# Performance work log

Measured on AMD Instinct MI355X. Metric: run time of the kernel, lower is better.

Reference implementation:

```python
import jax, jax.numpy as jnp
import numpy as np

N = 50000   # nodes per graph
E = 800000  # edges per graph
D = 128     # in_dim (num_features)
H = 128     # hidden_channels
R = 8       # num_etypes


def setup_inputs() -> dict:
    key = jax.random.key(0)
    ks = jax.random.split(key, 32)
    inp = {}
    inp["x1"] = jax.random.normal(ks[0], (N, D), dtype=jnp.float32)
    inp["edge_index1"] = jax.random.randint(ks[1], (2, E), 0, N)
    inp["edge_type1"] = jnp.sort(jax.random.randint(ks[2], (E,), 0, R))
    inp["x2"] = jax.random.normal(ks[3], (N, D), dtype=jnp.float32)
    inp["edge_index2"] = jax.random.randint(ks[4], (2, E), 0, N)
    inp["edge_type2"] = jnp.sort(jax.random.randint(ks[5], (E,), 0, R))
    # RGCNConv params: relation weights [R, in, out], root weight [in, out], bias [out]
    dims = [(D, H), (H, H), (H, H)]
    k = 6
    for l, (di, do) in enumerate(dims):
        s = 1.0 / np.sqrt(di)
        inp[f"W{l}"] = jax.random.normal(ks[k], (R, di, do), dtype=jnp.float32) * s; k += 1
        inp[f"root{l}"] = jax.random.normal(ks[k], (di, do), dtype=jnp.float32) * s; k += 1
        inp[f"bias{l}"] = jnp.zeros((do,), dtype=jnp.float32)
    # FCL: MLP on concat(u1, u2) of width 2*H -> H -> 1 (assumed architecture)
    s = 1.0 / np.sqrt(2 * H)
    inp["fc1_w"] = jax.random.normal(ks[k], (2 * H, H), dtype=jnp.float32) * s; k += 1
    inp["fc1_b"] = jnp.zeros((H,), dtype=jnp.float32)
    s = 1.0 / np.sqrt(H)
    inp["fc2_w"] = jax.random.normal(ks[k], (H, 1), dtype=jnp.float32) * s; k += 1
    inp["fc2_b"] = jnp.zeros((1,), dtype=jnp.float32)
    return inp


def rgcn_conv(x, src, dst, etype, W, root, bias):
    # PyG RGCNConv: out_i = root @ x_i + bias + sum_r mean_{j in N_r(i)} W_r x_j
    # transform all nodes by all relation weights: [R, N, H]
    t = jnp.einsum('nd,rdh->rnh', x, W)
    msg = t[etype, src]                       # [E, H] per-edge gathered messages
    comb = dst * R + etype                    # combined (node, relation) segment id
    cnt = jax.ops.segment_sum(jnp.ones((E,), x.dtype), comb, num_segments=N * R)
    msg = msg * (1.0 / jnp.maximum(cnt, 1.0))[comb][:, None]  # per-relation mean norm
    agg = jax.ops.segment_sum(msg, dst, num_segments=N)       # scatter-add over relations
    return agg + x @ root + bias


def gnn(x, edge_index, edge_type, params):
    src, dst = edge_index[0], edge_index[1]
    u = jax.nn.relu(rgcn_conv(x, src, dst, edge_type, *params[0]))
    u = jax.nn.relu(rgcn_conv(u, src, dst, edge_type, *params[1]))
    u = rgcn_conv(u, src, dst, edge_type, *params[2])
    return jnp.mean(u, axis=0).reshape(1, -1)  # [1, H]


def reference(x1, edge_index1, edge_type1, x2, edge_index2, edge_type2,
              W0, root0, bias0, W1, root1, bias1, W2, root2, bias2,
              fc1_w, fc1_b, fc2_w, fc2_b):
    params = [(W0, root0, bias0), (W1, root1, bias1), (W2, root2, bias2)]
    u1 = gnn(x1, edge_index1, edge_type1, params)
    u2 = gnn(x2, edge_index2, edge_type2, params)
    h = jnp.concatenate([u1, u2], axis=-1)    # [1, 2H]
    return jax.nn.relu(h @ fc1_w + fc1_b) @ fc2_w + fc2_b  # [1, 1]
```

## Files before the change

kernel.cpp:

```cpp
#include <hip/hip_runtime.h>

#define R_ET 8
#define DH 128

typedef __bf16 bf16x8 __attribute__((ext_vector_type(8)));
typedef float f32x4 __attribute__((ext_vector_type(4)));

__device__ __forceinline__ ushort f2bf(float f) {
  unsigned u = __float_as_uint(f);
  u += 0x7fff + ((u >> 16) & 1);
  return (ushort)(u >> 16);
}


__global__ void count_kernel(const int* __restrict__ ei, const int* __restrict__ et,
                             int* __restrict__ cnt, int E) {
  int e = blockIdx.x * blockDim.x + threadIdx.x;
  if (e < E) atomicAdd(&cnt[ei[E + e] * R_ET + et[e]], 1);
}

__global__ __launch_bounds__(1024) void scan1_kernel(const int* __restrict__ cnt,
                                                     int* __restrict__ off,
                                                     int* __restrict__ bsum, int N) {
  __shared__ int s[1024];
  int tid = threadIdx.x;
  int node = blockIdx.x * 1024 + tid;
  int d = 0;
  if (node < N) {
    const int4* c = (const int4*)&cnt[node * R_ET];
    int4 a = c[0], b = c[1];
    d = a.x + a.y + a.z + a.w + b.x + b.y + b.z + b.w;
  }
  s[tid] = d;
  __syncthreads();
  for (int step = 1; step < 1024; step <<= 1) {
    int v = (tid >= step) ? s[tid - step] : 0;
    __syncthreads();
    s[tid] += v;
    __syncthreads();
  }
  if (node < N) off[node] = s[tid] - d;
  if (tid == 1023) bsum[blockIdx.x] = s[1023];
}

__global__ __launch_bounds__(1024) void scan2_kernel(int* __restrict__ bsum, int nb) {
  __shared__ int s[1024];
  int tid = threadIdx.x;
  int v = (tid < nb) ? bsum[tid] : 0;
  s[tid] = v;
  __syncthreads();
  for (int step = 1; step < 1024; step <<= 1) {
    int x = (tid >= step) ? s[tid - step] : 0;
    __syncthreads();
    s[tid] += x;
    __syncthreads();
  }
  if (tid < nb) bsum[tid] = s[tid] - v;
}

__global__ __launch_bounds__(1024) void scan3_kernel(int* __restrict__ off,
                                                     int* __restrict__ cursor,
                                                     const int* __restrict__ bsum,
                                                     int N, int E) {
  int node = blockIdx.x * 1024 + threadIdx.x;
  if (node < N) {
    int o = off[node] + bsum[blockIdx.x];
    off[node] = o;
    cursor[node] = o;
  }
  if (node == 0) off[N] = E;
}

__global__ void place_kernel(const int* __restrict__ ei, const int* __restrict__ et,
                             const int* __restrict__ cnt, int* __restrict__ cursor,
                             int2* __restrict__ meta, int E) {
  int e = blockIdx.x * blockDim.x + threadIdx.x;
  if (e >= E) return;
  int src = ei[e], dst = ei[E + e], r = et[e];
  int slot = atomicAdd(&cursor[dst], 1);
  meta[slot] = make_int2(src | (r << 28),
                         __float_as_int(1.f / (float)cnt[dst * R_ET + r]));
}

__global__ __launch_bounds__(256) void wconv_kernel(const float* __restrict__ root,
                                                    const float* __restrict__ W,
                                                    ushort* __restrict__ Wt) {
  int mat = blockIdx.x;
  const float* src = (mat == 0) ? root : (W + (size_t)(mat - 1) * DH * DH);
  ushort* dst = Wt + (size_t)mat * DH * DH;
  for (int idx = threadIdx.x; idx < DH * DH; idx += 256) {
    int n = idx >> 7, k = idx & 127;
    dst[n * DH + (((k >> 3) ^ (n & 7)) << 3) + (k & 7)] = f2bf(src[k * DH + n]);
  }
}

__global__ __launch_bounds__(256) void aconv_kernel(const float* __restrict__ src,
                                                    ushort* __restrict__ dst,
                                                    int total, int padtotal) {
  int i4 = (blockIdx.x * 256 + threadIdx.x) * 4;
  if (i4 >= padtotal) return;
  int row = i4 >> 7, k = i4 & 127;
  ushort4 o = make_ushort4(0, 0, 0, 0);
  if (i4 < total) {
    float4 v = *(const float4*)&src[i4];
    o = make_ushort4(f2bf(v.x), f2bf(v.y), f2bf(v.z), f2bf(v.w));
  }
  *(ushort4*)&dst[(size_t)row * DH + (((k >> 3) ^ (row & 7)) << 3) + (k & 7)] = o;
}

__global__ __launch_bounds__(256) void gemm_mfma(
    const ushort* __restrict__ Abf, const ushort* __restrict__ Wt,
    const float* __restrict__ bias, float* __restrict__ y,
    ushort* __restrict__ t, int N) {
  __shared__ ushort As[128 * DH];
  __shared__ ushort Bs[128 * DH];
  const int tid = threadIdx.x;
  const int wave = tid >> 6, lane = tid & 63;
  const int quad = lane >> 4, l15 = lane & 15;
  const int rbase = blockIdx.x * 128;
  const int wr = (wave >> 1) * 64, wc = (wave & 1) * 64;

  const ushort* gA = Abf + (size_t)rbase * DH;
#pragma unroll
  for (int it = 0; it < 8; it++) {
    __builtin_amdgcn_global_load_lds(
        (const __attribute__((address_space(1))) void*)(gA + (it * 256 + tid) * 8),
        (__attribute__((address_space(3))) void*)(As + (it * 256 + wave * 64) * 8), 16, 0, 0);
  }
  {
    const ushort* gB = Wt + (size_t)(blockIdx.y * 3) * DH * DH;
#pragma unroll
    for (int it = 0; it < 8; it++) {
      __builtin_amdgcn_global_load_lds(
          (const __attribute__((address_space(1))) void*)(gB + (it * 256 + tid) * 8),
          (__attribute__((address_space(3))) void*)(Bs + (it * 256 + wave * 64) * 8), 16, 0, 0);
    }
  }

  for (int m = 0; m < 3; m++) {
    const int mat = blockIdx.y * 3 + m;
    __syncthreads();

    f32x4 acc[4][4];
#pragma unroll
    for (int i = 0; i < 4; i++)
#pragma unroll
      for (int j = 0; j < 4; j++) acc[i][j] = (f32x4){0.f, 0.f, 0.f, 0.f};

#pragma unroll
    for (int kc = 0; kc < 4; kc++) {
      bf16x8 af[4], bfr[4];
#pragma unroll
      for (int i = 0; i < 4; i++) {
        int ra = wr + i * 16 + l15;
        int rb = wc + i * 16 + l15;
        af[i] = *(const bf16x8*)&As[ra * DH + (((kc * 4 + quad) ^ (ra & 7)) << 3)];
        bfr[i] = *(const bf16x8*)&Bs[rb * DH + (((kc * 4 + quad) ^ (rb & 7)) << 3)];
      }
#pragma unroll
      for (int i = 0; i < 4; i++)
#pragma unroll
        for (int j = 0; j < 4; j++)
          acc[i][j] = __builtin_amdgcn_mfma_f32_16x16x32_bf16(bfr[j], af[i], acc[i][j], 0, 0, 0);
    }

    if (m < 2) {
      __syncthreads();
      const ushort* gB = Wt + (size_t)(mat + 1) * DH * DH;
#pragma unroll
      for (int it = 0; it < 8; it++) {
        __builtin_amdgcn_global_load_lds(
            (const __attribute__((address_space(1))) void*)(gB + (it * 256 + tid) * 8),
            (__attribute__((address_space(3))) void*)(Bs + (it * 256 + wave * 64) * 8), 16, 0, 0);
      }
    }

    if (mat == 0) {
#pragma unroll
      for (int i = 0; i < 4; i++) {
        int node = rbase + wr + i * 16 + l15;
        if (node < N) {
#pragma unroll
          for (int j = 0; j < 4; j++) {
            int c0 = wc + j * 16 + quad * 4;
            float4 bv = *(const float4*)&bias[c0];
            float4 v = make_float4(acc[i][j][0] + bv.x, acc[i][j][1] + bv.y,
                                   acc[i][j][2] + bv.z, acc[i][j][3] + bv.w);
            *(float4*)&y[(size_t)node * DH + c0] = v;
          }
        }
      }
    } else {
      ushort* tp = t + (size_t)(mat - 1) * (size_t)N * DH;
#pragma unroll
      for (int i = 0; i < 4; i++) {
        int node = rbase + wr + i * 16 + l15;
        if (node < N) {
#pragma unroll
          for (int j = 0; j < 4; j++) {
            int c0 = wc + j * 16 + quad * 4;
            unsigned lo = (unsigned)f2bf(acc[i][j][0]) | ((unsigned)f2bf(acc[i][j][1]) << 16);
            unsigned hi = (unsigned)f2bf(acc[i][j][2]) | ((unsigned)f2bf(acc[i][j][3]) << 16);
            *(uint2*)&tp[(size_t)node * DH + c0] = make_uint2(lo, hi);
          }
        }
      }
    }
  }
}

__device__ __forceinline__ void gather_accum(const int2* __restrict__ meta,
                                             const ushort* __restrict__ t,
                                             int start, int end, int lane, int N,
                                             float& ax, float& ay) {
  const int colb = lane * 2;
  for (int base = start; base < end; base += 64) {
    int m = min(64, end - base);
    int2 md = make_int2(0, 0);
    if (lane < m) md = meta[base + lane];
    int j = 0;
    for (; j + 4 <= m; j += 4) {
      int p0 = __shfl(md.x, j),     q0 = __shfl(md.y, j);
      int p1 = __shfl(md.x, j + 1), q1 = __shfl(md.y, j + 1);
      int p2 = __shfl(md.x, j + 2), q2 = __shfl(md.y, j + 2);
      int p3 = __shfl(md.x, j + 3), q3 = __shfl(md.y, j + 3);
      unsigned u0 = *(const unsigned*)&t[(((size_t)((unsigned)p0 >> 28) * N + (p0 & 0x0fffffff)) << 7) + colb];
      unsigned u1 = *(const unsigned*)&t[(((size_t)((unsigned)p1 >> 28) * N + (p1 & 0x0fffffff)) << 7) + colb];
      unsigned u2 = *(const unsigned*)&t[(((size_t)((unsigned)p2 >> 28) * N + (p2 & 0x0fffffff)) << 7) + colb];
      unsigned u3 = *(const unsigned*)&t[(((size_t)((unsigned)p3 >> 28) * N + (p3 & 0x0fffffff)) << 7) + colb];
      float s0 = __int_as_float(q0), s1 = __int_as_float(q1);
      float s2 = __int_as_float(q2), s3 = __int_as_float(q3);
      ax = fmaf(__uint_as_float(u0 << 16), s0, ax);
      ay = fmaf(__uint_as_float(u0 & 0xffff0000u), s0, ay);
      ax = fmaf(__uint_as_float(u1 << 16), s1, ax);
      ay = fmaf(__uint_as_float(u1 & 0xffff0000u), s1, ay);
      ax = fmaf(__uint_as_float(u2 << 16), s2, ax);
      ay = fmaf(__uint_as_float(u2 & 0xffff0000u), s2, ay);
      ax = fmaf(__uint_as_float(u3 << 16), s3, ax);
      ay = fmaf(__uint_as_float(u3 & 0xffff0000u), s3, ay);
    }
    for (; j < m; j++) {
      int pj = __shfl(md.x, j);
      float sj = __int_as_float(__shfl(md.y, j));
      unsigned u = *(const unsigned*)&t[(((size_t)((unsigned)pj >> 28) * N + (pj & 0x0fffffff)) << 7) + colb];
      ax = fmaf(__uint_as_float(u << 16), sj, ax);
      ay = fmaf(__uint_as_float(u & 0xffff0000u), sj, ay);
    }
  }
}

__global__ __launch_bounds__(256) void gather_mid(
    const int* __restrict__ off, const int2* __restrict__ meta,
    const ushort* __restrict__ t, const float* __restrict__ y,
    ushort* __restrict__ Abf, int N) {
  int dst = blockIdx.x * 4 + (threadIdx.x >> 6);
  if (dst >= N) return;
  int lane = threadIdx.x & 63;
  float ax = 0.f, ay = 0.f;
  gather_accum(meta, t, off[dst], off[dst + 1], lane, N, ax, ay);
  float2 yv = *(const float2*)&y[(size_t)dst * DH + lane * 2];
  float rx = fmaxf(yv.x + ax, 0.f);
  float ry = fmaxf(yv.y + ay, 0.f);
  unsigned o = (unsigned)f2bf(rx) | ((unsigned)f2bf(ry) << 16);
  int k = lane * 2;
  *(unsigned*)&Abf[(size_t)dst * DH + (((k >> 3) ^ (dst & 7)) << 3) + (k & 7)] = o;
}

__global__ __launch_bounds__(256) void gather_last(
    const int* __restrict__ off, const int2* __restrict__ meta,
    const ushort* __restrict__ t, float* __restrict__ y, int N) {
  int dst = blockIdx.x * 4 + (threadIdx.x >> 6);
  if (dst >= N) return;
  int lane = threadIdx.x & 63;
  float ax = 0.f, ay = 0.f;
  gather_accum(meta, t, off[dst], off[dst + 1], lane, N, ax, ay);
  float2* yp = (float2*)&y[(size_t)dst * DH + lane * 2];
  float2 yv = *yp;
  yv.x += ax;
  yv.y += ay;
  *yp = yv;
}

__global__ __launch_bounds__(256) void pool_kernel(const float* __restrict__ y,
                                                   float* __restrict__ u, int N) {
  __shared__ float s[256];
  int tid = threadIdx.x;
  int c = tid & 127, rr = tid >> 7;
  int n0 = blockIdx.x * 100;
  int nend = min(n0 + 100, N);
  float sum = 0.f;
  for (int n = n0 + rr; n < nend; n += 2) sum += y[(size_t)n * DH + c];
  s[tid] = sum;
  __syncthreads();
  if (tid < 128) atomicAdd(&u[c], s[tid] + s[tid + 128]);
}

__global__ __launch_bounds__(256) void mlp_kernel(
    const float* __restrict__ u, const float* __restrict__ fc1w,
    const float* __restrict__ fc1b, const float* __restrict__ fc2w,
    const float* __restrict__ fc2b, float* __restrict__ out, int N) {
  __shared__ float uin[256];
  __shared__ float hred[128];
  int tid = threadIdx.x;
  uin[tid] = u[tid] * (1.f / (float)N);
  __syncthreads();
  if (tid < 128) {
    float s = fc1b[tid];
    for (int i = 0; i < 256; i++) s = fmaf(uin[i], fc1w[i * 128 + tid], s);
    s = fmaxf(s, 0.f);
    hred[tid] = s * fc2w[tid];
  }
  __syncthreads();
  if (tid == 0) {
    float s = fc2b[0];
    for (int i = 0; i < 128; i++) s += hred[i];
    out[0] = s;
  }
}

extern "C" void kernel_launch(void* const* d_in, const int* in_sizes, int n_in,
                              void* d_out, int out_size, void* d_ws, size_t ws_size,
                              hipStream_t stream) {
  const float* x[2] = {(const float*)d_in[0], (const float*)d_in[3]};
  const int* ei[2] = {(const int*)d_in[1], (const int*)d_in[4]};
  const int* et[2] = {(const int*)d_in[2], (const int*)d_in[5]};
  const float* Wp[3] = {(const float*)d_in[6], (const float*)d_in[9], (const float*)d_in[12]};
  const float* rootp[3] = {(const float*)d_in[7], (const float*)d_in[10], (const float*)d_in[13]};
  const float* biasp[3] = {(const float*)d_in[8], (const float*)d_in[11], (const float*)d_in[14]};
  const float* fc1w = (const float*)d_in[15];
  const float* fc1b = (const float*)d_in[16];
  const float* fc2w = (const float*)d_in[17];
  const float* fc2b = (const float*)d_in[18];

  const int N = in_sizes[0] / DH;
  const int E = in_sizes[2];
  const int Npad = (N + 127) & ~127;
  const int NB = (N + 1023) / 1024;

  char* ws = (char*)d_ws;
  size_t ob = 0;
  auto alloc = [&](size_t bytes) {
    void* p = ws + ob;
    ob = (ob + bytes + 255) & ~(size_t)255;
    return p;
  };
  float* y = (float*)alloc((size_t)N * DH * 4);
  int* cnt = (int*)alloc((size_t)N * R_ET * 4);
  int* offs = (int*)alloc((size_t)(N + 1) * 4);
  int* cursor = (int*)alloc((size_t)N * 4);
  int* bsum = (int*)alloc(1024 * 4);
  int2* meta = (int2*)alloc((size_t)E * 8);
  float* u = (float*)alloc(1024);
  ushort* Abf = (ushort*)alloc((size_t)Npad * DH * 2);
  ushort* Wt = (ushort*)alloc((size_t)3 * 9 * DH * DH * 2);
  ushort* tbuf = (ushort*)alloc((size_t)R_ET * N * DH * 2);
  (void)ws_size;

  hipMemsetAsync(u, 0, 2 * DH * sizeof(float), stream);
  for (int l = 0; l < 3; l++)
    wconv_kernel<<<9, 256, 0, stream>>>(rootp[l], Wp[l], Wt + (size_t)l * 9 * DH * DH);

  dim3 ggrid(Npad / 128, 3);
  dim3 egrid((E + 255) / 256);
  dim3 ngrid((N + 3) / 4);
  const int total = N * DH, padtotal = Npad * DH;
  dim3 agrid((padtotal / 4 + 255) / 256);

  for (int g = 0; g < 2; g++) {
    hipMemsetAsync(cnt, 0, (size_t)N * R_ET * sizeof(int), stream);
    count_kernel<<<egrid, 256, 0, stream>>>(ei[g], et[g], cnt, E);
    scan1_kernel<<<NB, 1024, 0, stream>>>(cnt, offs, bsum, N);
    scan2_kernel<<<1, 1024, 0, stream>>>(bsum, NB);
    scan3_kernel<<<NB, 1024, 0, stream>>>(offs, cursor, bsum, N, E);
    place_kernel<<<egrid, 256, 0, stream>>>(ei[g], et[g], cnt, cursor, meta, E);
    aconv_kernel<<<agrid, 256, 0, stream>>>(x[g], Abf, total, padtotal);
    for (int l = 0; l < 3; l++) {
      gemm_mfma<<<ggrid, 256, 0, stream>>>(Abf, Wt + (size_t)l * 9 * DH * DH,
                                           biasp[l], y, tbuf, N);
      if (l < 2) {
        gather_mid<<<ngrid, 256, 0, stream>>>(offs, meta, tbuf, y, Abf, N);
      } else {
        gather_last<<<ngrid, 256, 0, stream>>>(offs, meta, tbuf, y, N);
      }
    }
    pool_kernel<<<(N + 99) / 100, 256, 0, stream>>>(y, u + g * DH, N);
  }
  mlp_kernel<<<1, 256, 0, stream>>>(u, fc1w, fc1b, fc2w, fc2b, (float*)d_out, N);
}
```

Before: 895.7 us.

## Build CSR with two-level bucket sort and fuse final gather with mean pooling

Replaces the per-(node,relation) global count, three-kernel scan and global-cursor placement with a coarse bucket count over 128-node buckets, a single-block scan, a coarse scatter, and a per-bucket shared-memory sort that also computes the per-relation mean normalisation. The last-layer gather now adds the root term and accumulates the pooled sum directly, removing the y write-back and the separate pool kernel. This reduces global atomics and launches for graph preprocessing but adds many global atomics onto 128 pooled addresses from every block.

```diff
diff --git a/kernel.cpp b/kernel.cpp
--- a/kernel.cpp
+++ b/kernel.cpp
@@ -13,73 +13,97 @@
 }
 
 
-__global__ void count_kernel(const int* __restrict__ ei, const int* __restrict__ et,
-                             int* __restrict__ cnt, int E) {
+
+__global__ void coarse_count(const int* __restrict__ ei, int* __restrict__ bcnt, int E) {
   int e = blockIdx.x * blockDim.x + threadIdx.x;
-  if (e < E) atomicAdd(&cnt[ei[E + e] * R_ET + et[e]], 1);
-}
-
-__global__ __launch_bounds__(1024) void scan1_kernel(const int* __restrict__ cnt,
-                                                     int* __restrict__ off,
-                                                     int* __restrict__ bsum, int N) {
+  if (e < E) atomicAdd(&bcnt[ei[E + e] >> 7], 1);
+}
+
+__global__ __launch_bounds__(1024) void coarse_scan(const int* __restrict__ bcnt,
+                                                    int* __restrict__ bbase,
+                                                    int* __restrict__ bcur,
+                                                    int nb, int E) {
   __shared__ int s[1024];
   int tid = threadIdx.x;
-  int node = blockIdx.x * 1024 + tid;
-  int d = 0;
-  if (node < N) {
-    const int4* c = (const int4*)&cnt[node * R_ET];
-    int4 a = c[0], b = c[1];
-    d = a.x + a.y + a.z + a.w + b.x + b.y + b.z + b.w;
-  }
-  s[tid] = d;
-  __syncthreads();
-  for (int step = 1; step < 1024; step <<= 1) {
-    int v = (tid >= step) ? s[tid - step] : 0;
-    __syncthreads();
-    s[tid] += v;
-    __syncthreads();
-  }
-  if (node < N) off[node] = s[tid] - d;
-  if (tid == 1023) bsum[blockIdx.x] = s[1023];
-}
-
-__global__ __launch_bounds__(1024) void scan2_kernel(int* __restrict__ bsum, int nb) {
-  __shared__ int s[1024];
-  int tid = threadIdx.x;
-  int v = (tid < nb) ? bsum[tid] : 0;
+  int v = (tid < nb) ? bcnt[tid] : 0;
   s[tid] = v;
   __syncthreads();
-  for (int step = 1; step < 1024; step <<= 1) {
-    int x = (tid >= step) ? s[tid - step] : 0;
+  for (int st = 1; st < 1024; st <<= 1) {
+    int x = (tid >= st) ? s[tid - st] : 0;
     __syncthreads();
     s[tid] += x;
     __syncthreads();
   }
-  if (tid < nb) bsum[tid] = s[tid] - v;
-}
-
-__global__ __launch_bounds__(1024) void scan3_kernel(int* __restrict__ off,
-                                                     int* __restrict__ cursor,
-                                                     const int* __restrict__ bsum,
-                                                     int N, int E) {
-  int node = blockIdx.x * 1024 + threadIdx.x;
-  if (node < N) {
-    int o = off[node] + bsum[blockIdx.x];
-    off[node] = o;
-    cursor[node] = o;
-  }
-  if (node == 0) off[N] = E;
-}
-
-__global__ void place_kernel(const int* __restrict__ ei, const int* __restrict__ et,
-                             const int* __restrict__ cnt, int* __restrict__ cursor,
-                             int2* __restrict__ meta, int E) {
+  if (tid < nb) {
+    bbase[tid] = s[tid] - v;
+    bcur[tid] = s[tid] - v;
+  }
+  if (tid == 0) bbase[nb] = E;
+}
+
+__global__ void coarse_place(const int* __restrict__ ei, const int* __restrict__ et,
+                             int* __restrict__ bcur, int* __restrict__ ebuf, int E) {
   int e = blockIdx.x * blockDim.x + threadIdx.x;
   if (e >= E) return;
   int src = ei[e], dst = ei[E + e], r = et[e];
-  int slot = atomicAdd(&cursor[dst], 1);
-  meta[slot] = make_int2(src | (r << 28),
-                         __float_as_int(1.f / (float)cnt[dst * R_ET + r]));
+  int slot = atomicAdd(&bcur[dst >> 7], 1);
+  ebuf[slot] = src | (r << 16) | ((dst & 127) << 19);
+}
+
+__global__ __launch_bounds__(256) void bucket_sort(
+    const int* __restrict__ bbase, const int* __restrict__ ebuf,
+    int2* __restrict__ meta, int* __restrict__ off, int N, int E) {
+  __shared__ int hist[1024];
+  __shared__ int cur[1024];
+  __shared__ float inv[1024];
+  __shared__ int tsum[256];
+  const int b = blockIdx.x, tid = threadIdx.x;
+  const int s0 = bbase[b], s1 = bbase[b + 1];
+
+  for (int k = tid; k < 1024; k += 256) hist[k] = 0;
+  __syncthreads();
+  for (int i = s0 + tid; i < s1; i += 256) {
+    int e = ebuf[i];
+    atomicAdd(&hist[(e >> 16) & 1023], 1);
+  }
+  __syncthreads();
+
+  const int base4 = tid * 4;
+  int h0 = hist[base4], h1 = hist[base4 + 1], h2 = hist[base4 + 2], h3 = hist[base4 + 3];
+  int s = h0 + h1 + h2 + h3;
+  tsum[tid] = s;
+  __syncthreads();
+  for (int st = 1; st < 256; st <<= 1) {
+    int x = (tid >= st) ? tsum[tid - st] : 0;
+    __syncthreads();
+    tsum[tid] += x;
+    __syncthreads();
+  }
+  int ex = tsum[tid] - s;
+  cur[base4] = ex;
+  cur[base4 + 1] = ex + h0;
+  cur[base4 + 2] = ex + h0 + h1;
+  cur[base4 + 3] = ex + h0 + h1 + h2;
+  inv[base4] = 1.f / (float)max(h0, 1);
+  inv[base4 + 1] = 1.f / (float)max(h1, 1);
+  inv[base4 + 2] = 1.f / (float)max(h2, 1);
+  inv[base4 + 3] = 1.f / (float)max(h3, 1);
+  __syncthreads();
+
+  if (tid < 128) {
+    int node = b * 128 + tid;
+    if (node < N) off[node] = s0 + cur[tid * 8];
+  }
+  if (b == gridDim.x - 1 && tid == 0) off[N] = E;
+  __syncthreads();
+
+  for (int i = s0 + tid; i < s1; i += 256) {
+    int e = ebuf[i];
+    int k = (e >> 16) & 1023;
+    int slot = s0 + atomicAdd(&cur[k], 1);
+    meta[slot] = make_int2((e & 0xffff) | (((e >> 16) & 7) << 28),
+                           __float_as_int(inv[k]));
+  }
 }
 
 __global__ __launch_bounds__(256) void wconv_kernel(const float* __restrict__ root,
@@ -266,33 +290,27 @@
   *(unsigned*)&Abf[(size_t)dst * DH + (((k >> 3) ^ (dst & 7)) << 3) + (k & 7)] = o;
 }
 
-__global__ __launch_bounds__(256) void gather_last(
+__global__ __launch_bounds__(256) void gather_last_pool(
     const int* __restrict__ off, const int2* __restrict__ meta,
-    const ushort* __restrict__ t, float* __restrict__ y, int N) {
-  int dst = blockIdx.x * 4 + (threadIdx.x >> 6);
-  if (dst >= N) return;
-  int lane = threadIdx.x & 63;
+    const ushort* __restrict__ t, const float* __restrict__ y,
+    float* __restrict__ u, int N) {
+  __shared__ float sb[128];
+  int tid = threadIdx.x;
+  if (tid < 128) sb[tid] = 0.f;
+  __syncthreads();
+  int dst = blockIdx.x * 4 + (tid >> 6);
+  int lane = tid & 63;
   float ax = 0.f, ay = 0.f;
-  gather_accum(meta, t, off[dst], off[dst + 1], lane, N, ax, ay);
-  float2* yp = (float2*)&y[(size_t)dst * DH + lane * 2];
-  float2 yv = *yp;
-  yv.x += ax;
-  yv.y += ay;
-  *yp = yv;
-}
-
-__global__ __launch_bounds__(256) void pool_kernel(const float* __restrict__ y,
-                                                   float* __restrict__ u, int N) {
-  __shared__ float s[256];
-  int tid = threadIdx.x;
-  int c = tid & 127, rr = tid >> 7;
-  int n0 = blockIdx.x * 100;
-  int nend = min(n0 + 100, N);
-  float sum = 0.f;
-  for (int n = n0 + rr; n < nend; n += 2) sum += y[(size_t)n * DH + c];
-  s[tid] = sum;
-  __syncthreads();
-  if (tid < 128) atomicAdd(&u[c], s[tid] + s[tid + 128]);
+  if (dst < N) {
+    gather_accum(meta, t, off[dst], off[dst + 1], lane, N, ax, ay);
+    float2 yv = *(const float2*)&y[(size_t)dst * DH + lane * 2];
+    ax += yv.x;
+    ay += yv.y;
+  }
+  atomicAdd(&sb[lane * 2], ax);
+  atomicAdd(&sb[lane * 2 + 1], ay);
+  __syncthreads();
+  if (tid < 128) atomicAdd(&u[tid], sb[tid]);
 }
 
 __global__ __launch_bounds__(256) void mlp_kernel(
@@ -321,6 +339,7 @@
 extern "C" void kernel_launch(void* const* d_in, const int* in_sizes, int n_in,
                               void* d_out, int out_size, void* d_ws, size_t ws_size,
                               hipStream_t stream) {
+  static_assert(R_ET <= 8, "ebuf packing assumes r fits in 3 bits");
   const float* x[2] = {(const float*)d_in[0], (const float*)d_in[3]};
   const int* ei[2] = {(const int*)d_in[1], (const int*)d_in[4]};
   const int* et[2] = {(const int*)d_in[2], (const int*)d_in[5]};
@@ -335,7 +354,7 @@
   const int N = in_sizes[0] / DH;
   const int E = in_sizes[2];
   const int Npad = (N + 127) & ~127;
-  const int NB = (N + 1023) / 1024;
+  const int nb = (N + 127) >> 7;
 
   char* ws = (char*)d_ws;
   size_t ob = 0;
@@ -345,10 +364,11 @@
     return p;
   };
   float* y = (float*)alloc((size_t)N * DH * 4);
-  int* cnt = (int*)alloc((size_t)N * R_ET * 4);
   int* offs = (int*)alloc((size_t)(N + 1) * 4);
-  int* cursor = (int*)alloc((size_t)N * 4);
-  int* bsum = (int*)alloc(1024 * 4);
+  int* bcnt = (int*)alloc(1024 * 4);
+  int* bbase = (int*)alloc(1028 * 4);
+  int* bcur = (int*)alloc(1024 * 4);
+  int* ebuf = (int*)alloc((size_t)E * 4);
   int2* meta = (int2*)alloc((size_t)E * 8);
   float* u = (float*)alloc(1024);
   ushort* Abf = (ushort*)alloc((size_t)Npad * DH * 2);
@@ -367,12 +387,11 @@
   dim3 agrid((padtotal / 4 + 255) / 256);
 
   for (int g = 0; g < 2; g++) {
-    hipMemsetAsync(cnt, 0, (size_t)N * R_ET * sizeof(int), stream);
-    count_kernel<<<egrid, 256, 0, stream>>>(ei[g], et[g], cnt, E);
-    scan1_kernel<<<NB, 1024, 0, stream>>>(cnt, offs, bsum, N);
-    scan2_kernel<<<1, 1024, 0, stream>>>(bsum, NB);
-    scan3_kernel<<<NB, 1024, 0, stream>>>(offs, cursor, bsum, N, E);
-    place_kernel<<<egrid, 256, 0, stream>>>(ei[g], et[g], cnt, cursor, meta, E);
+    hipMemsetAsync(bcnt, 0, nb * sizeof(int), stream);
+    coarse_count<<<egrid, 256, 0, stream>>>(ei[g], bcnt, E);
+    coarse_scan<<<1, 1024, 0, stream>>>(bcnt, bbase, bcur, nb, E);
+    coarse_place<<<egrid, 256, 0, stream>>>(ei[g], et[g], bcur, ebuf, E);
+    bucket_sort<<<nb, 256, 0, stream>>>(bbase, ebuf, meta, offs, N, E);
     aconv_kernel<<<agrid, 256, 0, stream>>>(x[g], Abf, total, padtotal);
     for (int l = 0; l < 3; l++) {
       gemm_mfma<<<ggrid, 256, 0, stream>>>(Abf, Wt + (size_t)l * 9 * DH * DH,
@@ -380,10 +399,9 @@
       if (l < 2) {
         gather_mid<<<ngrid, 256, 0, stream>>>(offs, meta, tbuf, y, Abf, N);
       } else {
-        gather_last<<<ngrid, 256, 0, stream>>>(offs, meta, tbuf, y, N);
+        gather_last_pool<<<ngrid, 256, 0, stream>>>(offs, meta, tbuf, y, u + g * DH, N);
       }
     }
-    pool_kernel<<<(N + 99) / 100, 256, 0, stream>>>(y, u + g * DH, N);
   }
   mlp_kernel<<<1, 256, 0, stream>>>(u, fc1w, fc1b, fc2w, fc2b, (float*)d_out, N);
 }
```

Measured after the change: 2.369 ms. 2.65x slower.
